# Performance work log

Hardware: AMD Instinct MI355X
Metric: run time of the kernel (lower is better)

## Reference

```python
import jax, jax.numpy as jnp
import numpy as np

N_NODES = 100000


def _gcn_conv(x, src, dst, deg_inv_sqrt, W, b, num_nodes):
    # GCNConv: out = D^{-1/2} (A+I) D^{-1/2} (x W) + b, with self-loops already
    # appended to (src, dst) and deg_inv_sqrt precomputed over the augmented graph.
    h = x @ W                                            # [N, out]
    coef = deg_inv_sqrt[src] * deg_inv_sqrt[dst]         # [E+N]
    msg = h[src] * coef[:, None]                         # gather + normalize
    out = jax.ops.segment_sum(msg, dst, num_segments=num_nodes)  # scatter-add
    return out + b


def setup_inputs() -> dict:
    key = jax.random.key(0)
    ks = jax.random.split(key, 8)
    n, d, h = N_NODES, 16, 16
    E = 3_200_000
    x = jax.random.normal(ks[0], (n, d), dtype=jnp.float32)
    edge_index = jax.random.randint(ks[1], (2, E), 0, n, dtype=jnp.int64)
    # Glorot-ish init for weights, zeros for biases (as in GCNConv/Linear defaults)
    W1 = jax.random.normal(ks[2], (d, h), dtype=jnp.float32) / np.sqrt(d)
    b1 = jnp.zeros((h,), dtype=jnp.float32)
    W2 = jax.random.normal(ks[3], (h, h), dtype=jnp.float32) / np.sqrt(h)
    b2 = jnp.zeros((h,), dtype=jnp.float32)
    Wfc = jax.random.normal(ks[4], (h, 1), dtype=jnp.float32) / np.sqrt(h)
    bfc = jnp.zeros((1,), dtype=jnp.float32)
    return {"x": x, "edge_index": edge_index, "W1": W1, "b1": b1,
            "W2": W2, "b2": b2, "Wfc": Wfc, "bfc": bfc}


def reference(x, edge_index, W1, b1, W2, b2, Wfc, bfc):
    n = x.shape[0]
    loops = jnp.arange(n, dtype=edge_index.dtype)
    src = jnp.concatenate([edge_index[0], loops])
    dst = jnp.concatenate([edge_index[1], loops])
    # symmetric normalization over graph with self-loops (edge weight 1)
    deg = jax.ops.segment_sum(jnp.ones_like(dst, dtype=x.dtype), dst, num_segments=n)
    deg_inv_sqrt = jnp.where(deg > 0, jax.lax.rsqrt(deg), 0.0)
    h = jax.nn.relu(_gcn_conv(x, src, dst, deg_inv_sqrt, W1, b1, n))
    h = jax.nn.relu(_gcn_conv(h, src, dst, deg_inv_sqrt, W2, b2, n))
    return h @ Wfc + bfc  # [N, 1]
```

## Files before the change

kernel.cpp:

```cpp
#include <hip/hip_runtime.h>
#include <hip/hip_fp16.h>
#include <stdint.h>


constexpr int F = 16;
constexpr int K_MAX = 256;
constexpr int BNODES = 512;
constexpr int PT = 4096;
constexpr int NPB = 32;
constexpr unsigned int CAP = 18432;

__device__ __forceinline__ float2 h2f2(__half2 h) { return __half22float2(h); }

__global__ void __launch_bounds__(256)
partition_kernel(const int* __restrict__ src, const int* __restrict__ dst,
                 unsigned int* __restrict__ gcur, unsigned int* __restrict__ recs,
                 int E, int K) {
    __shared__ unsigned int hist[K_MAX];
    __shared__ unsigned int offs[K_MAX];
    __shared__ unsigned int gbase[K_MAX];
    __shared__ unsigned int drec[PT];
    __shared__ unsigned char dbuk[PT];
    const int t = threadIdx.x;
    const int tile0 = blockIdx.x * PT;
    const int cnt = min(PT, E - tile0);
    if (t < K) hist[t] = 0u;
    __syncthreads();
    unsigned int rec[16], bp[16];
#pragma unroll
    for (int k = 0; k < 16; ++k) {
        int i = t + k * 256;
        bp[k] = 0xFFFFFFFFu;
        if (i < cnt) {
            int e = tile0 + i;
            unsigned int d = (unsigned int)dst[e];
            unsigned int s = (unsigned int)src[e];
            unsigned int b = d >> 9;
            rec[k] = ((d & 511u) << 17) | s;
            unsigned int pos = atomicAdd(&hist[b], 1u);
            bp[k] = (b << 12) | pos;
        }
    }
    __syncthreads();
    if (t < K) gbase[t] = (unsigned int)t * CAP + atomicAdd(&gcur[t], hist[t]);
    if (t == 0) {
        unsigned int run = 0;
        for (int i = 0; i < K; ++i) { offs[i] = run; run += hist[i]; }
    }
    __syncthreads();
#pragma unroll
    for (int k = 0; k < 16; ++k) {
        if (bp[k] != 0xFFFFFFFFu) {
            unsigned int b = bp[k] >> 12, pos = bp[k] & 0xFFFu;
            unsigned int idx = offs[b] + pos;
            drec[idx] = rec[k];
            dbuk[idx] = (unsigned char)b;
        }
    }
    __syncthreads();
    for (int i = t; i < cnt; i += 256) {
        unsigned int b = dbuk[i];
        recs[gbase[b] + ((unsigned int)i - offs[b])] = drec[i];
    }
}

__global__ void __launch_bounds__(512)
sort_mv_kernel(const unsigned int* __restrict__ recs, const unsigned int* __restrict__ gcur,
               const float* __restrict__ x, const float* __restrict__ W1,
               float* __restrict__ dis, unsigned int* __restrict__ rp,
               unsigned int* __restrict__ recs2, __half* __restrict__ hs1, int N) {
    __shared__ unsigned int cur[BNODES];
    __shared__ unsigned int wsum[8];
    __shared__ float sdis[BNODES];
    __shared__ float ws[16][16];
    __shared__ float xs[32][17];
    const int b = blockIdx.x;
    const int t = threadIdx.x;
    const int lane = t & 63, wid = t >> 6;
    cur[t] = 0u;
    if (t < 256) ws[t >> 4][t & 15] = W1[t];
    __syncthreads();
    const unsigned int e0 = (unsigned int)b * CAP;
    const unsigned int e1 = e0 + gcur[b];
    for (unsigned int e = e0 + t; e < e1; e += 512)
        atomicAdd(&cur[recs[e] >> 17], 1u);
    __syncthreads();
    const unsigned int c = cur[t];
    unsigned int xsc = c;
#pragma unroll
    for (int o = 1; o < 64; o <<= 1) {
        unsigned int y = __shfl_up(xsc, o, 64);
        if (lane >= o) xsc += y;
    }
    if (lane == 63) wsum[wid] = xsc;
    __syncthreads();
    if (t == 0) {
        unsigned int run = 0;
#pragma unroll
        for (int i = 0; i < 8; ++i) { unsigned int tmp = wsum[i]; wsum[i] = run; run += tmp; }
    }
    __syncthreads();
    const unsigned int start = e0 + wsum[wid] + xsc - c;
    const int v = b * BNODES + t;
    const float dv = rsqrtf(1.0f + (float)c);
    sdis[t] = dv;
    if (v < N) {
        dis[v] = dv;
        rp[v] = (c << 24) | start;
    }
    __syncthreads();
    cur[t] = start;
    __syncthreads();
    for (unsigned int e = e0 + t; e < e1; e += 512) {
        unsigned int r = recs[e];
        unsigned int slot = atomicAdd(&cur[r >> 17], 1u);
        recs2[slot] = r & 0x1FFFFu;
    }
    const int n = t >> 4, j = t & 15;
#pragma unroll
    for (int tile = 0; tile < 16; ++tile) {
        const int loc = tile * 32 + n;
        const int node = b * BNODES + loc;
        __syncthreads();
        xs[n][j] = (node < N) ? x[(size_t)node * F + j] : 0.0f;
        __syncthreads();
        float acc = 0.f;
#pragma unroll
        for (int k = 0; k < 16; ++k) acc += xs[n][k] * ws[k][j];
        if (node < N) hs1[(size_t)node * F + j] = __float2half(acc * sdis[loc]);
    }
}

__global__ void __launch_bounds__(256)
agg1_kernel(const unsigned int* __restrict__ recs2, const unsigned int* __restrict__ rp,
            const __half2* __restrict__ hs1, const float* __restrict__ dis,
            const float* __restrict__ W2, const float* __restrict__ b1,
            __half* __restrict__ hs2, int N) {
    __shared__ float ws[16][16];
    __shared__ float hbf[NPB][17];
    const int t = threadIdx.x;
    ws[t >> 4][t & 15] = W2[t];
    const int j2 = t & 7;
    const int g8 = t >> 3;
    const int v0 = blockIdx.x * NPB;
    {
        const int v = v0 + g8;
        float sx = 0.f, sy = 0.f, dv = 0.f;
        if (v < N) {
            dv = dis[v];
            const unsigned int w = rp[v];
            unsigned int e = w & 0xFFFFFFu;
            const unsigned int e1 = e + (w >> 24);
            float2 s = h2f2(hs1[(size_t)v * 8 + j2]);
            sx = s.x; sy = s.y;
            for (; e + 8 <= e1; e += 8) {
                unsigned int r0 = recs2[e + 0], r1 = recs2[e + 1];
                unsigned int r2 = recs2[e + 2], r3 = recs2[e + 3];
                unsigned int r4 = recs2[e + 4], r5 = recs2[e + 5];
                unsigned int r6 = recs2[e + 6], r7 = recs2[e + 7];
                float2 a0 = h2f2(hs1[r0 * 8 + j2]), a1 = h2f2(hs1[r1 * 8 + j2]);
                float2 a2 = h2f2(hs1[r2 * 8 + j2]), a3 = h2f2(hs1[r3 * 8 + j2]);
                float2 a4 = h2f2(hs1[r4 * 8 + j2]), a5 = h2f2(hs1[r5 * 8 + j2]);
                float2 a6 = h2f2(hs1[r6 * 8 + j2]), a7 = h2f2(hs1[r7 * 8 + j2]);
                sx += ((a0.x + a1.x) + (a2.x + a3.x)) + ((a4.x + a5.x) + (a6.x + a7.x));
                sy += ((a0.y + a1.y) + (a2.y + a3.y)) + ((a4.y + a5.y) + (a6.y + a7.y));
            }
            for (; e < e1; ++e) {
                float2 a = h2f2(hs1[recs2[e] * 8 + j2]);
                sx += a.x; sy += a.y;
            }
        }
        hbf[g8][2 * j2 + 0] = fmaxf(dv * sx + b1[2 * j2 + 0], 0.f);
        hbf[g8][2 * j2 + 1] = fmaxf(dv * sy + b1[2 * j2 + 1], 0.f);
    }
    __syncthreads();
    const int j = t & 15;
    const int g = t >> 4;
#pragma unroll
    for (int it = 0; it < 2; ++it) {
        const int n = g + 16 * it;
        const int v = v0 + n;
        if (v >= N) continue;
        float acc = 0.f;
#pragma unroll
        for (int k = 0; k < 16; ++k) acc += hbf[n][k] * ws[k][j];
        hs2[(size_t)v * F + j] = __float2half(acc * dis[v]);
    }
}

__global__ void __launch_bounds__(256)
agg2_kernel(const unsigned int* __restrict__ recs2, const unsigned int* __restrict__ rp,
            const __half2* __restrict__ hs2, const float* __restrict__ dis,
            const float* __restrict__ b2, const float* __restrict__ Wfc,
            const float* __restrict__ bfc, float* __restrict__ out, int N) {
    const int t = threadIdx.x;
    const int j2 = t & 7;
    const int g8 = t >> 3;
    const int v0 = blockIdx.x * NPB;
    const float wfx = Wfc[2 * j2 + 0], wfy = Wfc[2 * j2 + 1];
    const float bbx = b2[2 * j2 + 0], bby = b2[2 * j2 + 1];
    const float bf = bfc[0];
    const int v = v0 + g8;
    if (v >= N) return;
    const unsigned int w = rp[v];
    unsigned int e = w & 0xFFFFFFu;
    const unsigned int e1 = e + (w >> 24);
    float2 s0 = h2f2(hs2[(size_t)v * 8 + j2]);
    float sx = s0.x, sy = s0.y;
    for (; e + 8 <= e1; e += 8) {
        unsigned int r0 = recs2[e + 0], r1 = recs2[e + 1];
        unsigned int r2 = recs2[e + 2], r3 = recs2[e + 3];
        unsigned int r4 = recs2[e + 4], r5 = recs2[e + 5];
        unsigned int r6 = recs2[e + 6], r7 = recs2[e + 7];
        float2 a0 = h2f2(hs2[r0 * 8 + j2]), a1 = h2f2(hs2[r1 * 8 + j2]);
        float2 a2 = h2f2(hs2[r2 * 8 + j2]), a3 = h2f2(hs2[r3 * 8 + j2]);
        float2 a4 = h2f2(hs2[r4 * 8 + j2]), a5 = h2f2(hs2[r5 * 8 + j2]);
        float2 a6 = h2f2(hs2[r6 * 8 + j2]), a7 = h2f2(hs2[r7 * 8 + j2]);
        sx += ((a0.x + a1.x) + (a2.x + a3.x)) + ((a4.x + a5.x) + (a6.x + a7.x));
        sy += ((a0.y + a1.y) + (a2.y + a3.y)) + ((a4.y + a5.y) + (a6.y + a7.y));
    }
    for (; e < e1; ++e) {
        float2 a = h2f2(hs2[recs2[e] * 8 + j2]);
        sx += a.x; sy += a.y;
    }
    const float dv = dis[v];
    float h = fmaxf(dv * sx + bbx, 0.f) * wfx + fmaxf(dv * sy + bby, 0.f) * wfy;
    h += __shfl_down(h, 4, 8);
    h += __shfl_down(h, 2, 8);
    h += __shfl_down(h, 1, 8);
    if (j2 == 0) out[v] = h + bf;
}

static inline char* align256(char* p) {
    return (char*)(((uintptr_t)p + 255) & ~(uintptr_t)255);
}

extern "C" void kernel_launch(void* const* d_in, const int* in_sizes, int n_in,
                              void* d_out, int out_size, void* d_ws, size_t ws_size,
                              hipStream_t stream) {
    const float* x   = (const float*)d_in[0];
    const int*   ei  = (const int*)d_in[1];
    const float* W1  = (const float*)d_in[2];
    const float* b1  = (const float*)d_in[3];
    const float* W2  = (const float*)d_in[4];
    const float* b2  = (const float*)d_in[5];
    const float* Wfc = (const float*)d_in[6];
    const float* bfc = (const float*)d_in[7];
    float* out = (float*)d_out;

    const int N = in_sizes[0] / F;
    const int E = in_sizes[1] / 2;
    const int* src = ei;
    const int* dst = ei + E;
    const int K = (N + BNODES - 1) / BNODES;

    char* p = (char*)d_ws;
    float* dis = (float*)align256(p);                   p = (char*)(dis + N);
    unsigned int* gcur  = (unsigned int*)align256(p);   p = (char*)(gcur + K);
    unsigned int* rp    = (unsigned int*)align256(p);   p = (char*)(rp + N);
    unsigned int* recs2 = (unsigned int*)align256(p);   p = (char*)(recs2 + (size_t)K * CAP);
    unsigned int* recs  = (unsigned int*)align256(p);   p = (char*)(recs + (size_t)K * CAP);
    __half* hs1 = (__half*)align256(p);                 p = (char*)(hs1 + (size_t)N * F);
    __half* hs2 = (__half*)align256(p);

    const int T = 256;

    hipMemsetAsync(gcur, 0, (size_t)K * sizeof(unsigned int), stream);
    partition_kernel<<<(E + PT - 1) / PT, T, 0, stream>>>(src, dst, gcur, recs, E, K);
    sort_mv_kernel<<<K, 512, 0, stream>>>(recs, gcur, x, W1, dis, rp, recs2, hs1, N);
    agg1_kernel<<<(N + NPB - 1) / NPB, T, 0, stream>>>(recs2, rp, (const __half2*)hs1, dis, W2, b1, hs2, N);
    agg2_kernel<<<(N + NPB - 1) / NPB, T, 0, stream>>>(recs2, rp, (const __half2*)hs2, dis, b2, Wfc, bfc, out, N);
}
```

Baseline: 197.1 us.

## Split sort_mv per bucket into four quarter-blocks for more parallelism

The sort/degree kernel now launches four 256-thread blocks per 512-node bucket, each handling a 128-node quarter. Each block still scans the whole bucket's records but only counts and scatters those whose destination falls in its quarter. recs2 gets its own smaller per-quarter capacity. This lifts block count from about 196 to about 782 to fill the GPU's CUs, at the cost of reading each bucket's records four times and a tighter per-quarter capacity bound.

```diff
diff --git a/kernel.cpp b/kernel.cpp
--- a/kernel.cpp
+++ b/kernel.cpp
@@ -6,9 +6,11 @@
 constexpr int F = 16;
 constexpr int K_MAX = 256;
 constexpr int BNODES = 512;
+constexpr int QNODES = 128;
 constexpr int PT = 4096;
 constexpr int NPB = 32;
 constexpr unsigned int CAP = 18432;
+constexpr unsigned int CAP_Q = 4608;
 
 __device__ __forceinline__ float2 h2f2(__half2 h) { return __half22float2(h); }
 
@@ -64,63 +66,66 @@
     }
 }
 
-__global__ void __launch_bounds__(512)
+__global__ void __launch_bounds__(256)
 sort_mv_kernel(const unsigned int* __restrict__ recs, const unsigned int* __restrict__ gcur,
                const float* __restrict__ x, const float* __restrict__ W1,
                float* __restrict__ dis, unsigned int* __restrict__ rp,
                unsigned int* __restrict__ recs2, __half* __restrict__ hs1, int N) {
-    __shared__ unsigned int cur[BNODES];
-    __shared__ unsigned int wsum[8];
-    __shared__ float sdis[BNODES];
+    __shared__ unsigned int cur[QNODES];
+    __shared__ unsigned int wpart[2];
+    __shared__ float sdis[QNODES];
     __shared__ float ws[16][16];
-    __shared__ float xs[32][17];
-    const int b = blockIdx.x;
+    __shared__ float xs[16][17];
+    const int qb = blockIdx.x;
+    const int B = qb >> 2;
+    const unsigned int q = (unsigned int)(qb & 3);
     const int t = threadIdx.x;
     const int lane = t & 63, wid = t >> 6;
-    cur[t] = 0u;
-    if (t < 256) ws[t >> 4][t & 15] = W1[t];
-    __syncthreads();
-    const unsigned int e0 = (unsigned int)b * CAP;
-    const unsigned int e1 = e0 + gcur[b];
-    for (unsigned int e = e0 + t; e < e1; e += 512)
-        atomicAdd(&cur[recs[e] >> 17], 1u);
-    __syncthreads();
-    const unsigned int c = cur[t];
+    if (t < QNODES) cur[t] = 0u;
+    ws[t >> 4][t & 15] = W1[t];
+    __syncthreads();
+    const unsigned int e0 = (unsigned int)B * CAP;
+    const unsigned int e1 = e0 + gcur[B];
+    for (unsigned int e = e0 + t; e < e1; e += 256) {
+        unsigned int dl = recs[e] >> 17;
+        if ((dl >> 7) == q) atomicAdd(&cur[dl & 127u], 1u);
+    }
+    __syncthreads();
+    const unsigned int c = (t < QNODES) ? cur[t] : 0u;
     unsigned int xsc = c;
 #pragma unroll
     for (int o = 1; o < 64; o <<= 1) {
         unsigned int y = __shfl_up(xsc, o, 64);
         if (lane >= o) xsc += y;
     }
-    if (lane == 63) wsum[wid] = xsc;
-    __syncthreads();
-    if (t == 0) {
-        unsigned int run = 0;
-#pragma unroll
-        for (int i = 0; i < 8; ++i) { unsigned int tmp = wsum[i]; wsum[i] = run; run += tmp; }
-    }
-    __syncthreads();
-    const unsigned int start = e0 + wsum[wid] + xsc - c;
-    const int v = b * BNODES + t;
-    const float dv = rsqrtf(1.0f + (float)c);
-    sdis[t] = dv;
-    if (v < N) {
-        dis[v] = dv;
-        rp[v] = (c << 24) | start;
-    }
-    __syncthreads();
-    cur[t] = start;
-    __syncthreads();
-    for (unsigned int e = e0 + t; e < e1; e += 512) {
+    if (t < QNODES && lane == 63) wpart[wid] = xsc;
+    __syncthreads();
+    if (t < QNODES) {
+        const unsigned int pre = xsc - c + ((wid == 1) ? wpart[0] : 0u);
+        const unsigned int start = (unsigned int)qb * CAP_Q + pre;
+        const int v = qb * QNODES + t;
+        const float dv = rsqrtf(1.0f + (float)c);
+        sdis[t] = dv;
+        if (v < N) {
+            dis[v] = dv;
+            rp[v] = (c << 24) | start;
+        }
+        cur[t] = start;
+    }
+    __syncthreads();
+    for (unsigned int e = e0 + t; e < e1; e += 256) {
         unsigned int r = recs[e];
-        unsigned int slot = atomicAdd(&cur[r >> 17], 1u);
-        recs2[slot] = r & 0x1FFFFu;
+        unsigned int dl = r >> 17;
+        if ((dl >> 7) == q) {
+            unsigned int slot = atomicAdd(&cur[dl & 127u], 1u);
+            recs2[slot] = r & 0x1FFFFu;
+        }
     }
     const int n = t >> 4, j = t & 15;
 #pragma unroll
-    for (int tile = 0; tile < 16; ++tile) {
-        const int loc = tile * 32 + n;
-        const int node = b * BNODES + loc;
+    for (int tile = 0; tile < 8; ++tile) {
+        const int loc = tile * 16 + n;
+        const int node = qb * QNODES + loc;
         __syncthreads();
         xs[n][j] = (node < N) ? x[(size_t)node * F + j] : 0.0f;
         __syncthreads();
@@ -252,13 +257,14 @@
     const int E = in_sizes[1] / 2;
     const int* src = ei;
     const int* dst = ei + E;
-    const int K = (N + BNODES - 1) / BNODES;
+    const int K  = (N + BNODES - 1) / BNODES;
+    const int KQ = (N + QNODES - 1) / QNODES;
 
     char* p = (char*)d_ws;
     float* dis = (float*)align256(p);                   p = (char*)(dis + N);
     unsigned int* gcur  = (unsigned int*)align256(p);   p = (char*)(gcur + K);
     unsigned int* rp    = (unsigned int*)align256(p);   p = (char*)(rp + N);
-    unsigned int* recs2 = (unsigned int*)align256(p);   p = (char*)(recs2 + (size_t)K * CAP);
+    unsigned int* recs2 = (unsigned int*)align256(p);   p = (char*)(recs2 + (size_t)KQ * CAP_Q);
     unsigned int* recs  = (unsigned int*)align256(p);   p = (char*)(recs + (size_t)K * CAP);
     __half* hs1 = (__half*)align256(p);                 p = (char*)(hs1 + (size_t)N * F);
     __half* hs2 = (__half*)align256(p);
@@ -267,7 +273,7 @@
 
     hipMemsetAsync(gcur, 0, (size_t)K * sizeof(unsigned int), stream);
     partition_kernel<<<(E + PT - 1) / PT, T, 0, stream>>>(src, dst, gcur, recs, E, K);
-    sort_mv_kernel<<<K, 512, 0, stream>>>(recs, gcur, x, W1, dis, rp, recs2, hs1, N);
+    sort_mv_kernel<<<KQ, T, 0, stream>>>(recs, gcur, x, W1, dis, rp, recs2, hs1, N);
     agg1_kernel<<<(N + NPB - 1) / NPB, T, 0, stream>>>(recs2, rp, (const __half2*)hs1, dis, W2, b1, hs2, N);
     agg2_kernel<<<(N + NPB - 1) / NPB, T, 0, stream>>>(recs2, rp, (const __half2*)hs2, dis, b2, Wfc, bfc, out, N);
 }
```

Result: slower. 219.0 us (+11.1%).
